# Performance work log

Measured on AMD Instinct MI355X. Metric: run time of the kernel, lower is better.

## Reference

```python
import jax, jax.numpy as jnp
import numpy as np

NEG_FILL = -1000000.0


def setup_inputs() -> dict:
    key = jax.random.key(0)
    k1, k2, k3, k4, k5 = jax.random.split(key, 5)
    bs, sl, hd, dd = 128, 512, 1024, 512
    x = jax.random.normal(k1, (bs, sl, hd), dtype=jnp.float32)
    mask = jax.random.randint(k2, (bs, sl), 0, 2) > 0  # bool, True = masked out
    Wq = jax.random.normal(k3, (dd, hd), dtype=jnp.float32)
    bq = jax.random.normal(k4, (dd,), dtype=jnp.float32)
    vq = jax.random.normal(k5, (dd,), dtype=jnp.float32)
    return {"x": x, "mask": mask, "Wq": Wq, "bq": bq, "vq": vq}


def reference(x, mask, Wq, bq, vq):
    # key = tanh(Uq(x)): [bs, sl, dd]
    k = jnp.tanh(jnp.einsum("bsh,dh->bsd", x, Wq) + bq)
    # score = vq . key: [bs, sl]
    score = jnp.einsum("bsd,d->bs", k, vq)
    score = jnp.where(mask, NEG_FILL, score)
    weight = jax.nn.softmax(score, axis=-1)  # [bs, sl]
    # weighted sum over sequence: [bs, hd]
    res = jnp.einsum("bs,bsh->bh", weight, x)
    return res
```

## Files before the change

kernel.cpp:

```cpp
#include <hip/hip_runtime.h>
#include <stdint.h>

#define BS 128
#define SL 512
#define HD 1024
#define DD 512
#define M_TOT (BS*SL)

typedef __attribute__((ext_vector_type(8))) short short8;
typedef __attribute__((ext_vector_type(4))) float f32x4;

__device__ __forceinline__ unsigned short f32_bf16(float f) {
    union { float f; unsigned u; } v; v.f = f;
    unsigned u = v.u + 0x7FFFu + ((v.u >> 16) & 1u);
    return (unsigned short)(u >> 16);
}
__device__ __forceinline__ float bf16_f32(unsigned short h) {
    union { unsigned u; float f; } v; v.u = ((unsigned)h) << 16; return v.f;
}
__device__ __forceinline__ float u2f(unsigned u) {
    union { unsigned u; float f; } v; v.u = u; return v.f;
}
__device__ __forceinline__ unsigned cvt_pk_bf16(float a, float b) {
    unsigned r;
    asm("v_cvt_pk_bf16_f32 %0, %1, %2" : "=v"(r) : "v"(a), "v"(b));
    return r;
}
__device__ __forceinline__ float fast_tanh(float x) {
    float e = __expf(2.0f * x);
    return 1.0f - 2.0f / (e + 1.0f);
}
__device__ __forceinline__ void async_lds16(const void* g, void* l) {
    __builtin_amdgcn_global_load_lds(
        (const __attribute__((address_space(1))) unsigned int*)g,
        (__attribute__((address_space(3))) unsigned int*)l, 16, 0, 0);
}

__global__ void pack_wq_kernel(const float* __restrict__ Wq,
                               unsigned short* __restrict__ P,
                               const unsigned* __restrict__ mw,
                               int* __restrict__ flag) {
    if (blockIdx.x == 0) {
        unsigned bad = 0;
        for (int i = threadIdx.x; i < 1024; i += 256) bad |= (mw[i] > 1u) ? 1u : 0u;
        if (bad) atomicExch(flag, 1);
    }
    int t = blockIdx.x * 256 + threadIdx.x;
    int d  = t >> 7;
    int h0 = (t & 127) << 3;
    const float* src = Wq + (size_t)d * HD + h0;
    union { unsigned short s[8]; uint4 v; } a, b;
#pragma unroll
    for (int j = 0; j < 8; ++j) {
        float f = src[j];
        a.s[j] = f32_bf16(f);
        b.s[j] = f32_bf16(f - bf16_f32(a.s[j]));
    }
    int nb = d >> 7, cg = (d >> 4) & 7, lr = d & 15;
    int ks = h0 >> 5, q = (h0 >> 3) & 3;
    int l = q * 16 + lr;
    size_t base = (size_t)(nb * 32 + ks) * 8192 + (size_t)(cg * 64 + l) * 8;
    *(uint4*)(P + base)        = a.v;
    *(uint4*)(P + base + 4096) = b.v;
}

__launch_bounds__(256, 3)
__global__ void score_kernel(const float* __restrict__ x,
                             const unsigned short* __restrict__ packW,
                             const float* __restrict__ bq,
                             const float* __restrict__ vq,
                             float* __restrict__ score) {
    __shared__ unsigned short A_hi[4096];
    __shared__ unsigned short A_lo[4096];
    __shared__ unsigned short Bt[2][8192];

    const int bid = blockIdx.x;
    const int xcd = bid & 7;
    const int slot = bid >> 3;
    const int nb = slot & 3;
    const int m0 = (xcd + ((slot >> 2) << 3)) << 7;

    const int t = threadIdx.x;
    const int l = t & 63;
    const int w = t >> 6;
    const int wm = w & 1, wn = w >> 1;

    f32x4 acc[4][4];
#pragma unroll
    for (int i = 0; i < 4; ++i)
#pragma unroll
        for (int j = 0; j < 4; ++j)
            acc[i][j] = (f32x4){0.f, 0.f, 0.f, 0.f};

    const char* Ahc = (const char*)A_hi;
    const char* Alc = (const char*)A_lo;

    float4 px[2][2];
    {
        const unsigned short* src = packW + (size_t)(nb * 32) * 8192;
#pragma unroll
        for (int r = 0; r < 4; ++r)
            async_lds16(src + (size_t)(r * 256 + t) * 8,
                        (unsigned short*)Bt[0] + (r * 256 + t) * 8);
    }
    __builtin_amdgcn_sched_barrier(0);
#pragma unroll
    for (int r = 0; r < 2; ++r) {
        int u = r * 256 + t;
        int row = u >> 2, c8 = u & 3;
        const float4* xp = (const float4*)(x + (size_t)(m0 + row) * HD + c8 * 8);
        px[r][0] = xp[0]; px[r][1] = xp[1];
    }

    for (int ks = 0; ks < 32; ++ks) {
        const int cur = ks & 1;
        if (ks < 31) {
            const unsigned short* src = packW + (size_t)(nb * 32 + ks + 1) * 8192;
#pragma unroll
            for (int r = 0; r < 4; ++r)
                async_lds16(src + (size_t)(r * 256 + t) * 8,
                            (unsigned short*)Bt[cur ^ 1] + (r * 256 + t) * 8);
        }
        __builtin_amdgcn_sched_barrier(0);
#pragma unroll
        for (int r = 0; r < 2; ++r) {
            int u = r * 256 + t;
            int row = u >> 2, c8 = u & 3;
            int rg = row >> 4, rr = row & 15;
            int off = (((rg * 64 + c8 * 16 + rr) * 16) ^ (c8 << 5));
            float4 v0 = px[r][0], v1 = px[r][1];
            unsigned h0 = cvt_pk_bf16(v0.x, v0.y);
            unsigned h1 = cvt_pk_bf16(v0.z, v0.w);
            unsigned h2 = cvt_pk_bf16(v1.x, v1.y);
            unsigned h3 = cvt_pk_bf16(v1.z, v1.w);
            unsigned l0 = cvt_pk_bf16(v0.x - u2f(h0 << 16), v0.y - u2f(h0 & 0xFFFF0000u));
            unsigned l1 = cvt_pk_bf16(v0.z - u2f(h1 << 16), v0.w - u2f(h1 & 0xFFFF0000u));
            unsigned l2 = cvt_pk_bf16(v1.x - u2f(h2 << 16), v1.y - u2f(h2 & 0xFFFF0000u));
            unsigned l3 = cvt_pk_bf16(v1.z - u2f(h3 << 16), v1.w - u2f(h3 & 0xFFFF0000u));
            uint4 hv = {h0, h1, h2, h3};
            uint4 lv = {l0, l1, l2, l3};
            *(uint4*)((char*)A_hi + off) = hv;
            *(uint4*)((char*)A_lo + off) = lv;
        }
        if (ks < 31) {
#pragma unroll
            for (int r = 0; r < 2; ++r) {
                int u = r * 256 + t;
                int row = u >> 2, c8 = u & 3;
                const float4* xp = (const float4*)(x + (size_t)(m0 + row) * HD
                                                   + (ks + 1) * 32 + c8 * 8);
                px[r][0] = xp[0]; px[r][1] = xp[1];
            }
        }
        __builtin_amdgcn_sched_barrier(0);
        asm volatile("s_waitcnt lgkmcnt(0)" ::: "memory");
        __builtin_amdgcn_s_barrier();

        const short8* Bh = (const short8*)Bt[cur];
        const short8* Bl = (const short8*)(Bt[cur] + 4096);
        short8 ah[4], al[4], bh[4], bl[4];
        const int xr = (l >> 4) << 5;
#pragma unroll
        for (int i = 0; i < 4; ++i) {
            int off = ((((wm * 4 + i) * 64 + l) * 16) ^ xr);
            ah[i] = *(const short8*)(Ahc + off);
            al[i] = *(const short8*)(Alc + off);
        }
#pragma unroll
        for (int j = 0; j < 4; ++j) {
            bh[j] = Bh[(wn * 4 + j) * 64 + l];
            bl[j] = Bl[(wn * 4 + j) * 64 + l];
        }
#pragma unroll
        for (int i = 0; i < 4; ++i)
#pragma unroll
            for (int j = 0; j < 4; ++j) {
                acc[i][j] = __builtin_amdgcn_mfma_f32_16x16x32_bf16(ah[i], bh[j], acc[i][j], 0, 0, 0);
                acc[i][j] = __builtin_amdgcn_mfma_f32_16x16x32_bf16(al[i], bh[j], acc[i][j], 0, 0, 0);
                acc[i][j] = __builtin_amdgcn_mfma_f32_16x16x32_bf16(ah[i], bl[j], acc[i][j], 0, 0, 0);
            }

        __builtin_amdgcn_s_barrier();
    }

    int q = l >> 4, c = l & 15;
#pragma unroll
    for (int i = 0; i < 4; ++i) {
        float rs[4] = {0.f, 0.f, 0.f, 0.f};
#pragma unroll
        for (int j = 0; j < 4; ++j) {
            int n = nb * 128 + wn * 64 + j * 16 + c;
            float bqv = bq[n], vqv = vq[n];
            f32x4 a4 = acc[i][j];
#pragma unroll
            for (int r = 0; r < 4; ++r)
                rs[r] += fast_tanh(a4[r] + bqv) * vqv;
        }
#pragma unroll
        for (int r = 0; r < 4; ++r) {
            float v = rs[r];
            v += __shfl_xor(v, 1);
            v += __shfl_xor(v, 2);
            v += __shfl_xor(v, 4);
            v += __shfl_xor(v, 8);
            if (c == 0)
                atomicAdd(&score[m0 + wm * 64 + i * 16 + q * 4 + r], v);
        }
    }
}

__global__ void attend_kernel(const float* __restrict__ x,
                              const float* __restrict__ score,
                              const void* __restrict__ maskp,
                              const int* __restrict__ flag,
                              float* __restrict__ out) {
    __shared__ float red[8];
    __shared__ float wsh[SL];
    __shared__ int   lst[64];
    __shared__ float wlst[64];
    __shared__ int   cntS;
    int b = blockIdx.x, sc = blockIdx.y, t = threadIdx.x;
    int w = t >> 6;
    bool u8 = (*flag != 0);
    int i0 = b * SL + t, i1 = i0 + 256;
    bool mk0, mk1;
    if (u8) {
        mk0 = ((const unsigned char*)maskp)[i0] != 0;
        mk1 = ((const unsigned char*)maskp)[i1] != 0;
    } else {
        mk0 = ((const int*)maskp)[i0] != 0;
        mk1 = ((const int*)maskp)[i1] != 0;
    }
    float s0 = mk0 ? -1000000.0f : score[i0];
    float s1 = mk1 ? -1000000.0f : score[i1];
    float mx = fmaxf(s0, s1);
    for (int d = 1; d < 64; d <<= 1) mx = fmaxf(mx, __shfl_xor(mx, d));
    if ((t & 63) == 0) red[w] = mx;
    __syncthreads();
    mx = fmaxf(fmaxf(red[0], red[1]), fmaxf(red[2], red[3]));
    float e0 = expf(s0 - mx), e1 = expf(s1 - mx);
    float sm = e0 + e1;
    for (int d = 1; d < 64; d <<= 1) sm += __shfl_xor(sm, d);
    if ((t & 63) == 0) red[4 + w] = sm;
    __syncthreads();
    sm = red[4] + red[5] + red[6] + red[7];
    float inv = 1.0f / sm;
    wsh[t] = e0 * inv;
    wsh[t + 256] = e1 * inv;
    __syncthreads();

    if (t < 64) {
        float wv = wsh[sc * 64 + t];
        bool nz = (wv != 0.0f);
        unsigned long long m = __ballot(nz);
        int pos = __popcll(m & ((1ULL << t) - 1ULL));
        if (nz) { lst[pos] = t; wlst[pos] = wv; }
        if (t == 0) cntS = (int)__popcll(m);
    }
    __syncthreads();
    int cnt = cntS;

    const float4* xb = (const float4*)(x + ((size_t)b * SL + sc * 64) * HD) + t;
    float ax = 0.f, ay = 0.f, az = 0.f, aw = 0.f;
#pragma unroll 4
    for (int s = 0; s < cnt; ++s) {
        int row = lst[s];
        float wv = wlst[s];
        float4 v = xb[(size_t)row * 256];
        ax += wv * v.x; ay += wv * v.y; az += wv * v.z; aw += wv * v.w;
    }
    float* op = out + (size_t)b * HD + t * 4;
    atomicAdd(op + 0, ax);
    atomicAdd(op + 1, ay);
    atomicAdd(op + 2, az);
    atomicAdd(op + 3, aw);
}

extern "C" void kernel_launch(void* const* d_in, const int* in_sizes, int n_in,
                              void* d_out, int out_size, void* d_ws, size_t ws_size,
                              hipStream_t stream) {
    const float* x  = (const float*)d_in[0];
    const void* mask = d_in[1];
    const float* Wq = (const float*)d_in[2];
    const float* bq = (const float*)d_in[3];
    const float* vq = (const float*)d_in[4];
    float* out = (float*)d_out;

    char* ws = (char*)d_ws;
    unsigned short* packW = (unsigned short*)ws;
    float* score   = (float*)(ws + (2u << 20));
    int*   flag    = (int*)  (ws + (2u << 20) + (256u << 10));

    hipMemsetAsync(score, 0, (256u << 10) + 4, stream);
    hipMemsetAsync(out, 0, (size_t)BS * HD * sizeof(float), stream);

    pack_wq_kernel<<<256, 256, 0, stream>>>(Wq, packW, (const unsigned*)mask, flag);
    score_kernel<<<2048, 256, 0, stream>>>(x, packW, bq, vq, score);
    attend_kernel<<<dim3(BS, 8), 256, 0, stream>>>(x, score, mask, flag, out);
}
```

Measured before the change: 510.5 us.

## Single-buffer low-bf16 weight tile to cut LDS and raise occupancy to four blocks

The combined hi/lo weight double buffer is split so only the high bf16 half stays double-buffered, and the low half is single-buffered and loaded within the current iteration. This cuts LDS per block from 48KB to 40KB and raises launch bounds from 3 to 4 blocks per CU. The wait is now an explicit vmcnt count so only the current low tile and earlier loads must have landed. In exchange, the low-part load sits on the critical path each iteration, and register pressure under the tighter launch bound may cause spills.

```diff
diff --git a/kernel.cpp b/kernel.cpp
--- a/kernel.cpp
+++ b/kernel.cpp
@@ -64,7 +64,7 @@
     *(uint4*)(P + base + 4096) = b.v;
 }
 
-__launch_bounds__(256, 3)
+__launch_bounds__(256, 4)
 __global__ void score_kernel(const float* __restrict__ x,
                              const unsigned short* __restrict__ packW,
                              const float* __restrict__ bq,
@@ -72,7 +72,8 @@
                              float* __restrict__ score) {
     __shared__ unsigned short A_hi[4096];
     __shared__ unsigned short A_lo[4096];
-    __shared__ unsigned short Bt[2][8192];
+    __shared__ unsigned short Bhi[2][4096];
+    __shared__ unsigned short Blo[4096];
 
     const int bid = blockIdx.x;
     const int xcd = bid & 7;
@@ -99,9 +100,9 @@
     {
         const unsigned short* src = packW + (size_t)(nb * 32) * 8192;
 #pragma unroll
-        for (int r = 0; r < 4; ++r)
+        for (int r = 0; r < 2; ++r)
             async_lds16(src + (size_t)(r * 256 + t) * 8,
-                        (unsigned short*)Bt[0] + (r * 256 + t) * 8);
+                        (unsigned short*)Bhi[0] + (r * 256 + t) * 8);
     }
     __builtin_amdgcn_sched_barrier(0);
 #pragma unroll
@@ -114,12 +115,20 @@
 
     for (int ks = 0; ks < 32; ++ks) {
         const int cur = ks & 1;
+        {
+            const unsigned short* srcl = packW + (size_t)(nb * 32 + ks) * 8192 + 4096;
+#pragma unroll
+            for (int r = 0; r < 2; ++r)
+                async_lds16(srcl + (size_t)(r * 256 + t) * 8,
+                            (unsigned short*)Blo + (r * 256 + t) * 8);
+        }
+        __builtin_amdgcn_sched_barrier(0);
         if (ks < 31) {
-            const unsigned short* src = packW + (size_t)(nb * 32 + ks + 1) * 8192;
-#pragma unroll
-            for (int r = 0; r < 4; ++r)
-                async_lds16(src + (size_t)(r * 256 + t) * 8,
-                            (unsigned short*)Bt[cur ^ 1] + (r * 256 + t) * 8);
+            const unsigned short* srch = packW + (size_t)(nb * 32 + ks + 1) * 8192;
+#pragma unroll
+            for (int r = 0; r < 2; ++r)
+                async_lds16(srch + (size_t)(r * 256 + t) * 8,
+                            (unsigned short*)Bhi[cur ^ 1] + (r * 256 + t) * 8);
         }
         __builtin_amdgcn_sched_barrier(0);
 #pragma unroll
@@ -153,11 +162,14 @@
             }
         }
         __builtin_amdgcn_sched_barrier(0);
-        asm volatile("s_waitcnt lgkmcnt(0)" ::: "memory");
+        if (ks < 31)
+            asm volatile("s_waitcnt vmcnt(6) lgkmcnt(0)" ::: "memory");
+        else
+            asm volatile("s_waitcnt vmcnt(0) lgkmcnt(0)" ::: "memory");
         __builtin_amdgcn_s_barrier();
 
-        const short8* Bh = (const short8*)Bt[cur];
-        const short8* Bl = (const short8*)(Bt[cur] + 4096);
+        const short8* Bh = (const short8*)Bhi[cur];
+        const short8* Bl8 = (const short8*)Blo;
         short8 ah[4], al[4], bh[4], bl[4];
         const int xr = (l >> 4) << 5;
 #pragma unroll
@@ -169,7 +181,7 @@
 #pragma unroll
         for (int j = 0; j < 4; ++j) {
             bh[j] = Bh[(wn * 4 + j) * 64 + l];
-            bl[j] = Bl[(wn * 4 + j) * 64 + l];
+            bl[j] = Bl8[(wn * 4 + j) * 64 + l];
         }
 #pragma unroll
         for (int i = 0; i < 4; ++i)
```

After: 1.124 ms. 120% more time.

## Load A fragments directly from global into registers, bypassing LDS staging

Applied to the files above, without the earlier changes.

The x tile is no longer converted and written to shared memory and then read back as MFMA fragments. Each wave now loads its own rows of x straight into the MFMA register layout and splits them into bf16 hi/lo in registers. The aim is to remove the LDS stores, the LDS reads and the lgkmcnt wait for the A operand, and to free shared memory. In exchange, both waves that share the same rows load those rows and repeat the hi/lo conversion, which doubles A global traffic and conversion work and adds register pressure.

```diff
diff --git a/kernel.cpp b/kernel.cpp
--- a/kernel.cpp
+++ b/kernel.cpp
@@ -70,8 +70,6 @@
                              const float* __restrict__ bq,
                              const float* __restrict__ vq,
                              float* __restrict__ score) {
-    __shared__ unsigned short A_hi[4096];
-    __shared__ unsigned short A_lo[4096];
     __shared__ unsigned short Bt[2][8192];
 
     const int bid = blockIdx.x;
@@ -92,10 +90,10 @@
         for (int j = 0; j < 4; ++j)
             acc[i][j] = (f32x4){0.f, 0.f, 0.f, 0.f};
 
-    const char* Ahc = (const char*)A_hi;
-    const char* Alc = (const char*)A_lo;
-
-    float4 px[2][2];
+    const int arow = wm * 64 + (l & 15);
+    const int acol = (l >> 4) << 3;
+
+    float4 px[4][2];
     {
         const unsigned short* src = packW + (size_t)(nb * 32) * 8192;
 #pragma unroll
@@ -105,10 +103,8 @@
     }
     __builtin_amdgcn_sched_barrier(0);
 #pragma unroll
-    for (int r = 0; r < 2; ++r) {
-        int u = r * 256 + t;
-        int row = u >> 2, c8 = u & 3;
-        const float4* xp = (const float4*)(x + (size_t)(m0 + row) * HD + c8 * 8);
+    for (int r = 0; r < 4; ++r) {
+        const float4* xp = (const float4*)(x + (size_t)(m0 + arow + r * 16) * HD + acol);
         px[r][0] = xp[0]; px[r][1] = xp[1];
     }
 
@@ -122,12 +118,9 @@
                             (unsigned short*)Bt[cur ^ 1] + (r * 256 + t) * 8);
         }
         __builtin_amdgcn_sched_barrier(0);
-#pragma unroll
-        for (int r = 0; r < 2; ++r) {
-            int u = r * 256 + t;
-            int row = u >> 2, c8 = u & 3;
-            int rg = row >> 4, rr = row & 15;
-            int off = (((rg * 64 + c8 * 16 + rr) * 16) ^ (c8 << 5));
+        short8 ah[4], al[4];
+#pragma unroll
+        for (int r = 0; r < 4; ++r) {
             float4 v0 = px[r][0], v1 = px[r][1];
             unsigned h0 = cvt_pk_bf16(v0.x, v0.y);
             unsigned h1 = cvt_pk_bf16(v0.z, v0.w);
@@ -137,35 +130,26 @@
             unsigned l1 = cvt_pk_bf16(v0.z - u2f(h1 << 16), v0.w - u2f(h1 & 0xFFFF0000u));
             unsigned l2 = cvt_pk_bf16(v1.x - u2f(h2 << 16), v1.y - u2f(h2 & 0xFFFF0000u));
             unsigned l3 = cvt_pk_bf16(v1.z - u2f(h3 << 16), v1.w - u2f(h3 & 0xFFFF0000u));
-            uint4 hv = {h0, h1, h2, h3};
-            uint4 lv = {l0, l1, l2, l3};
-            *(uint4*)((char*)A_hi + off) = hv;
-            *(uint4*)((char*)A_lo + off) = lv;
-        }
+            union { unsigned u[4]; short8 s; } H, L;
+            H.u[0] = h0; H.u[1] = h1; H.u[2] = h2; H.u[3] = h3;
+            L.u[0] = l0; L.u[1] = l1; L.u[2] = l2; L.u[3] = l3;
+            ah[r] = H.s; al[r] = L.s;
+        }
+        __builtin_amdgcn_sched_barrier(0);
         if (ks < 31) {
 #pragma unroll
-            for (int r = 0; r < 2; ++r) {
-                int u = r * 256 + t;
-                int row = u >> 2, c8 = u & 3;
-                const float4* xp = (const float4*)(x + (size_t)(m0 + row) * HD
-                                                   + (ks + 1) * 32 + c8 * 8);
+            for (int r = 0; r < 4; ++r) {
+                const float4* xp = (const float4*)(x + (size_t)(m0 + arow + r * 16) * HD
+                                                   + (ks + 1) * 32 + acol);
                 px[r][0] = xp[0]; px[r][1] = xp[1];
             }
         }
         __builtin_amdgcn_sched_barrier(0);
-        asm volatile("s_waitcnt lgkmcnt(0)" ::: "memory");
         __builtin_amdgcn_s_barrier();
 
         const short8* Bh = (const short8*)Bt[cur];
         const short8* Bl = (const short8*)(Bt[cur] + 4096);
-        short8 ah[4], al[4], bh[4], bl[4];
-        const int xr = (l >> 4) << 5;
-#pragma unroll
-        for (int i = 0; i < 4; ++i) {
-            int off = ((((wm * 4 + i) * 64 + l) * 16) ^ xr);
-            ah[i] = *(const short8*)(Ahc + off);
-            al[i] = *(const short8*)(Alc + off);
-        }
+        short8 bh[4], bl[4];
 #pragma unroll
         for (int j = 0; j < 4; ++j) {
             bh[j] = Bh[(wn * 4 + j) * 64 + l];
```

Result: slower. 613.4 us (+20.2%).
